# Kernel optimization log

Measured on AMD Instinct MI355X. Metric: run time of the kernel, lower is better.

The kernel has to match this reference:

```python
import jax, jax.numpy as jnp
import numpy as np

N, DIM = 100000, 512
HID = DIM // 2


def _mlp(z, W1, b1, W2, b2):
    # shared scorer: [N, dim] -> [N, 1]
    h = jax.nn.relu(z @ W1 + b1)
    return h @ W2 + b2


def setup_inputs() -> dict:
    key = jax.random.key(0)
    k1, k2, k3, k4 = jax.random.split(key, 4)
    s1 = 1.0 / np.sqrt(DIM)
    s2 = 1.0 / np.sqrt(HID)
    return {
        "z1": jax.random.normal(k1, (N, DIM), dtype=jnp.float32),
        "z2": jax.random.normal(k2, (N, DIM), dtype=jnp.float32),
        "W1": jax.random.normal(k3, (DIM, HID), dtype=jnp.float32) * s1,
        "b1": jnp.zeros((HID,), dtype=jnp.float32),
        "W2": jax.random.normal(k4, (HID, 1), dtype=jnp.float32) * s2,
        "b2": jnp.zeros((1,), dtype=jnp.float32),
    }


def reference(z1, z2, W1, b1, W2, b2):
    x = _mlp(z1, W1, b1, W2, b2)  # [N, 1]
    y = _mlp(z2, W1, b1, W2, b2)  # [N, 1]
    # exp-normalize pair: score_x = e^x / (e^x + e^y) == sigmoid(x - y)
    # computed exactly as in the original (plain exp, no max-subtract)
    e_x = jnp.exp(x)
    e_y = jnp.exp(y)
    denom = e_x + e_y
    score_x = e_x / denom  # [N, 1]
    score_y = e_y / denom  # [N, 1]
    # diag(score) @ z  ==  score * z  (row-wise broadcast scale)
    return score_x * z1 + score_y * z2
```

## Files before the change

### kernel.cpp

```cpp
#include <hip/hip_runtime.h>
#include <hip/hip_bf16.h>
#include <cmath>

#define DIM 512
#define HID 256
#define ROWS_PB 32
#define NCHUNK 16
#define CB 16384

typedef __attribute__((ext_vector_type(8))) short short8;
typedef __attribute__((ext_vector_type(4))) float f32x4;
typedef __attribute__((ext_vector_type(4))) unsigned int u32x4;

__device__ __forceinline__ unsigned short f2bf(float f) {
  union { float f; unsigned u; } v; v.f = f;
  unsigned u = v.u;
  return (unsigned short)((u + 0x7FFFu + ((u >> 16) & 1u)) >> 16);
}
__device__ __forceinline__ float bf2f(short h) {
  union { unsigned u; float f; } v;
  v.u = ((unsigned)(unsigned short)h) << 16;
  return v.f;
}

__global__ void w1_swz_kernel(const float* __restrict__ W1,
                              unsigned short* __restrict__ w1s) {
  int tid = blockIdx.x * blockDim.x + threadIdx.x;
  if (tid >= DIM * HID) return;
  int k = tid / HID;
  int c = tid - k * HID;
  w1s[(((k >> 3) * HID) + c) * 8 + (k & 7)] = f2bf(W1[tid]);
}

__device__ __forceinline__ short8 cvt8(const f32x4 p0, const f32x4 p1) {
  short8 r;
  r[0] = (short)f2bf(p0[0]); r[1] = (short)f2bf(p0[1]);
  r[2] = (short)f2bf(p0[2]); r[3] = (short)f2bf(p0[3]);
  r[4] = (short)f2bf(p1[0]); r[5] = (short)f2bf(p1[1]);
  r[6] = (short)f2bf(p1[2]); r[7] = (short)f2bf(p1[3]);
  return r;
}

__device__ __forceinline__ void wcombine(float wa, const short8 a, float wb,
                                         const short8 b, f32x4& o0, f32x4& o1) {
#pragma unroll
  for (int i = 0; i < 4; ++i) {
    o0[i] = wa * bf2f(a[i]) + wb * bf2f(b[i]);
    o1[i] = wa * bf2f(a[i + 4]) + wb * bf2f(b[i + 4]);
  }
}

__global__ __launch_bounds__(256, 2) void fa_main_kernel(
    const float* __restrict__ z1, const float* __restrict__ z2,
    const unsigned short* __restrict__ w1s,
    const float* __restrict__ bias1, const float* __restrict__ W2,
    const float* __restrict__ bias2, float* __restrict__ out, int n) {
  __shared__ char smem[81920];
  short8* Az = (short8*)smem;
  char* Bs = smem + 65536;
  float* xs = (float*)(smem + 65536);

  const int t = threadIdx.x;
  const int w = t >> 6;
  const int l = t & 63;
  const int l15 = l & 15, l16 = l >> 4;
  const int s = w & 1;
  const int tl = w >> 1;
  const int row0 = blockIdx.x * ROWS_PB;
  const int myrow = row0 + tl * 16 + l15;
  const bool rok = myrow < n;
  const float* zz = s ? z2 : z1;
  const float* ap = zz + (size_t)myrow * DIM + (l16 << 3);
  const f32x4 zf4 = (f32x4){0.f, 0.f, 0.f, 0.f};

  u32x4 breg0, breg1, breg2, breg3;
#define BLOAD(c)                                            \
  {                                                         \
    const u32x4* g = (const u32x4*)w1s + (c) * 1024 + t;    \
    breg0 = g[0];                                           \
    breg1 = g[256];                                         \
    breg2 = g[512];                                         \
    breg3 = g[768];                                         \
  }
#define BWRITE()                                            \
  {                                                         \
    u32x4* d = (u32x4*)Bs + t;                              \
    d[0] = breg0;                                           \
    d[256] = breg1;                                         \
    d[512] = breg2;                                         \
    d[768] = breg3;                                         \
  }

  BLOAD(0);
  __builtin_amdgcn_sched_barrier(0);
#pragma unroll
  for (int g = 0; g < 4; ++g) {
    f32x4 p[4][2];
#pragma unroll
    for (int j = 0; j < 4; ++j) {
      const float* pp = ap + (((g << 2) + j) << 5);
      p[j][0] = rok ? *(const f32x4*)(pp) : zf4;
      p[j][1] = rok ? *(const f32x4*)(pp + 4) : zf4;
    }
#pragma unroll
    for (int j = 0; j < 4; ++j)
      Az[((s * NCHUNK + (g << 2) + j) * 2 + tl) * 64 + l] =
          cvt8(p[j][0], p[j][1]);
  }
  BWRITE();
  __syncthreads();

  f32x4 acc[16];
#pragma unroll
  for (int f = 0; f < 16; ++f) acc[f] = zf4;

#pragma unroll
  for (int c = 0; c < NCHUNK; ++c) {
    if (c + 1 < NCHUNK) BLOAD(c + 1);
    __builtin_amdgcn_sched_barrier(0);
    const short8* bp = (const short8*)Bs + (l16 << 8) + l15;
    const short8 af = Az[((s * NCHUNK + c) * 2 + tl) * 64 + l];
    short8 bf[16];
#pragma unroll
    for (int f = 0; f < 16; ++f) bf[f] = bp[f << 4];
    __builtin_amdgcn_sched_barrier(0);
#pragma unroll
    for (int f = 0; f < 16; ++f)
      acc[f] =
          __builtin_amdgcn_mfma_f32_16x16x32_bf16(af, bf[f], acc[f], 0, 0, 0);
    __syncthreads();
    if (c + 1 < NCHUNK) BWRITE();
    __syncthreads();
  }

  float part[4] = {0.f, 0.f, 0.f, 0.f};
#pragma unroll
  for (int f = 0; f < 16; ++f) {
    const int cc = (f << 4) + l15;
    const float w2v = W2[cc];
    const float b1v = bias1[cc];
#pragma unroll
    for (int r = 0; r < 4; ++r) {
      const float hh = acc[f][r] + b1v;
      part[r] += (hh > 0.f) ? hh * w2v : 0.f;
    }
  }
#pragma unroll
  for (int r = 0; r < 4; ++r) {
#pragma unroll
    for (int m = 1; m < 16; m <<= 1) part[r] += __shfl_xor(part[r], m, 16);
  }
  if (l15 == 0) {
#pragma unroll
    for (int r = 0; r < 4; ++r)
      xs[s * ROWS_PB + tl * 16 + (l16 << 2) + r] = part[r];
  }
  __syncthreads();

  const float x = xs[tl * 16 + l15];
  const float y = xs[ROWS_PB + tl * 16 + l15];
  const float sx = 1.f / (1.f + __expf(y - x));
  const float sy = 1.f - sx;
  float* orow = out + (size_t)myrow * DIM + (l16 << 3);
  if (rok) {
#pragma unroll
    for (int j = 0; j < 8; ++j) {
      const int cc = (s << 3) + j;
      const short8 a0 = Az[((0 * NCHUNK + cc) * 2 + tl) * 64 + l];
      const short8 a1 = Az[((1 * NCHUNK + cc) * 2 + tl) * 64 + l];
      f32x4 o0, o1;
      wcombine(sx, a0, sy, a1, o0, o1);
      *(f32x4*)(orow + (cc << 5)) = o0;
      *(f32x4*)(orow + (cc << 5) + 4) = o1;
    }
  }
#undef BLOAD
#undef BWRITE
}

extern "C" void kernel_launch(void* const* d_in, const int* in_sizes, int n_in,
                              void* d_out, int out_size, void* d_ws,
                              size_t ws_size, hipStream_t stream) {
  const float* z1 = (const float*)d_in[0];
  const float* z2 = (const float*)d_in[1];
  const float* W1 = (const float*)d_in[2];
  const float* b1 = (const float*)d_in[3];
  const float* W2 = (const float*)d_in[4];
  const float* b2 = (const float*)d_in[5];
  float* out = (float*)d_out;
  const int n = in_sizes[0] / DIM;
  unsigned short* w1s = (unsigned short*)d_ws;

  hipLaunchKernelGGL(w1_swz_kernel, dim3((DIM * HID + 255) / 256), dim3(256),
                     0, stream, W1, w1s);
  const int nwg = (n + ROWS_PB - 1) / ROWS_PB;
  hipLaunchKernelGGL(fa_main_kernel, dim3(nwg), dim3(256), 0, stream, z1, z2,
                     w1s, b1, W2, b2, out, n);
}
```

Baseline: 187.2 us.

## Switch GEMM to 32x32x16 MFMA with per-wave hidden-column split

```diff
diff --git a/kernel.cpp b/kernel.cpp
--- a/kernel.cpp
+++ b/kernel.cpp
@@ -10,6 +10,7 @@
 
 typedef __attribute__((ext_vector_type(8))) short short8;
 typedef __attribute__((ext_vector_type(4))) float f32x4;
+typedef __attribute__((ext_vector_type(16))) float f32x16;
 typedef __attribute__((ext_vector_type(4))) unsigned int u32x4;
 
 __device__ __forceinline__ unsigned short f2bf(float f) {
@@ -58,16 +59,17 @@
   __shared__ char smem[81920];
   short8* Az = (short8*)smem;
   char* Bs = smem + 65536;
-  float* xs = (float*)(smem + 65536);
+  float* xs2 = (float*)(smem + 65536);
 
   const int t = threadIdx.x;
   const int w = t >> 6;
   const int l = t & 63;
   const int l15 = l & 15, l16 = l >> 4;
+  const int l31 = l & 31, lhi = l >> 5;
   const int s = w & 1;
-  const int tl = w >> 1;
+  const int h = w >> 1;
   const int row0 = blockIdx.x * ROWS_PB;
-  const int myrow = row0 + tl * 16 + l15;
+  const int myrow = row0 + h * 16 + l15;
   const bool rok = myrow < n;
   const float* zz = s ? z2 : z1;
   const float* ap = zz + (size_t)myrow * DIM + (l16 << 3);
@@ -104,70 +106,86 @@
     }
 #pragma unroll
     for (int j = 0; j < 4; ++j)
-      Az[((s * NCHUNK + (g << 2) + j) * 2 + tl) * 64 + l] =
+      Az[((s * NCHUNK + (g << 2) + j) * 2 + h) * 64 + l] =
           cvt8(p[j][0], p[j][1]);
   }
   BWRITE();
   __syncthreads();
 
-  f32x4 acc[16];
-#pragma unroll
-  for (int f = 0; f < 16; ++f) acc[f] = zf4;
+  f32x16 acc[4];
+#pragma unroll
+  for (int g = 0; g < 4; ++g)
+#pragma unroll
+    for (int r = 0; r < 16; ++r) acc[g][r] = 0.f;
+
+  const int aTl = (l31 >> 4);
+  const int aLo = (l & 15);
+  const int bBase = (h << 2) * 32 + l31;
 
 #pragma unroll
   for (int c = 0; c < NCHUNK; ++c) {
     if (c + 1 < NCHUNK) BLOAD(c + 1);
     __builtin_amdgcn_sched_barrier(0);
-    const short8* bp = (const short8*)Bs + (l16 << 8) + l15;
-    const short8 af = Az[((s * NCHUNK + c) * 2 + tl) * 64 + l];
-    short8 bf[16];
-#pragma unroll
-    for (int f = 0; f < 16; ++f) bf[f] = bp[f << 4];
-    __builtin_amdgcn_sched_barrier(0);
-#pragma unroll
-    for (int f = 0; f < 16; ++f)
-      acc[f] =
-          __builtin_amdgcn_mfma_f32_16x16x32_bf16(af, bf[f], acc[f], 0, 0, 0);
+    const short8* azc = Az + ((s * NCHUNK + c) * 2 + aTl) * 64 + aLo;
+    const short8* bsc = (const short8*)Bs;
+#pragma unroll
+    for (int ks = 0; ks < 2; ++ks) {
+      const short8 af = azc[((ks << 1) + lhi) << 4];
+      const short8* bp = bsc + (((ks << 1) + lhi) << 8) + bBase;
+#pragma unroll
+      for (int g = 0; g < 4; ++g) {
+        const short8 bf = bp[g << 5];
+        acc[g] = __builtin_amdgcn_mfma_f32_32x32x16_bf16(af, bf, acc[g], 0, 0,
+                                                         0);
+      }
+    }
     __syncthreads();
     if (c + 1 < NCHUNK) BWRITE();
     __syncthreads();
   }
 
-  float part[4] = {0.f, 0.f, 0.f, 0.f};
-#pragma unroll
-  for (int f = 0; f < 16; ++f) {
-    const int cc = (f << 4) + l15;
+  float part[16];
+#pragma unroll
+  for (int r = 0; r < 16; ++r) part[r] = 0.f;
+#pragma unroll
+  for (int g = 0; g < 4; ++g) {
+    const int cc = ((h << 2) + g) * 32 + l31;
     const float w2v = W2[cc];
     const float b1v = bias1[cc];
 #pragma unroll
-    for (int r = 0; r < 4; ++r) {
-      const float hh = acc[f][r] + b1v;
+    for (int r = 0; r < 16; ++r) {
+      const float hh = acc[g][r] + b1v;
       part[r] += (hh > 0.f) ? hh * w2v : 0.f;
     }
   }
 #pragma unroll
-  for (int r = 0; r < 4; ++r) {
-#pragma unroll
-    for (int m = 1; m < 16; m <<= 1) part[r] += __shfl_xor(part[r], m, 16);
-  }
-  if (l15 == 0) {
-#pragma unroll
-    for (int r = 0; r < 4; ++r)
-      xs[s * ROWS_PB + tl * 16 + (l16 << 2) + r] = part[r];
+  for (int r = 0; r < 16; ++r) {
+#pragma unroll
+    for (int m = 1; m < 32; m <<= 1) part[r] += __shfl_xor(part[r], m, 64);
+  }
+  if (l31 == 0) {
+#pragma unroll
+    for (int r = 0; r < 16; ++r) {
+      const int row = (r & 3) + ((r >> 2) << 3) + (lhi << 2);
+      xs2[(s * 2 + h) * 32 + row] = part[r];
+    }
   }
   __syncthreads();
 
-  const float x = xs[tl * 16 + l15];
-  const float y = xs[ROWS_PB + tl * 16 + l15];
+  const int tl2 = w & 1;
+  const int orow_l = tl2 * 16 + l15;
+  const int grow = row0 + orow_l;
+  const float x = xs2[0 * 32 + orow_l] + xs2[1 * 32 + orow_l];
+  const float y = xs2[2 * 32 + orow_l] + xs2[3 * 32 + orow_l];
   const float sx = 1.f / (1.f + __expf(y - x));
   const float sy = 1.f - sx;
-  float* orow = out + (size_t)myrow * DIM + (l16 << 3);
-  if (rok) {
+  float* orow = out + (size_t)grow * DIM + (l16 << 3);
+  if (grow < n) {
 #pragma unroll
     for (int j = 0; j < 8; ++j) {
-      const int cc = (s << 3) + j;
-      const short8 a0 = Az[((0 * NCHUNK + cc) * 2 + tl) * 64 + l];
-      const short8 a1 = Az[((1 * NCHUNK + cc) * 2 + tl) * 64 + l];
+      const int cc = ((w >> 1) << 3) + j;
+      const short8 a0 = Az[((0 * NCHUNK + cc) * 2 + tl2) * 64 + l];
+      const short8 a1 = Az[((1 * NCHUNK + cc) * 2 + tl2) * 64 + l];
       f32x4 o0, o1;
       wcombine(sx, a0, sy, a1, o0, o1);
       *(f32x4*)(orow + (cc << 5)) = o0;
```

Result: slower. 200.4 us (+7.1%).
